# Kernel tuning notes

Hardware: AMD Instinct MI355X
Metric: run time of the kernel (lower is better)

Reference implementation:

```python
import jax, jax.numpy as jnp
import numpy as np

DICT_LEN = 9
NUM_LS = 8
DIM = 1024
SEQ = 2048
BZ = 32


def setup_inputs() -> dict:
    key = jax.random.key(0)
    k_x, k_ids, k_w, k_b = jax.random.split(key, 4)
    x = jax.random.normal(k_x, (SEQ, BZ, DIM), dtype=jnp.float32)
    lang_ids = jax.random.randint(k_ids, (BZ,), 0, DICT_LEN)
    # torch nn.Linear init: U(-1/sqrt(in), 1/sqrt(in)), weight shape [out, in]
    bound = 1.0 / np.sqrt(DIM)
    W = jax.random.uniform(k_w, (NUM_LS, DIM, DIM), dtype=jnp.float32, minval=-bound, maxval=bound)
    b = jax.random.uniform(k_b, (NUM_LS, DIM), dtype=jnp.float32, minval=-bound, maxval=bound)
    return {"x": x, "lang_ids": lang_ids, "W": W, "b": b}


def reference(x, lang_ids, W, b):
    # Mapper.forward: gid = dict_len - 1 - lang_ids; tokens with gid in [1, num_ls]
    # are transformed by Linear #(gid-1); all other batch columns pass through.
    gid = DICT_LEN - 1 - lang_ids                      # [bz]
    active = (gid >= 1) & (gid <= NUM_LS)              # [bz]
    eidx = jnp.clip(gid - 1, 0, NUM_LS - 1)            # [bz] expert index (dummy 0 where inactive)
    We = W[eidx]                                       # [bz, dim, dim] (torch Linear weight layout [out, in])
    be = b[eidx]                                       # [bz, dim]
    y = jnp.einsum("sbd,bed->sbe", x, We) + be[None, :, :]
    return jnp.where(active[None, :, None], y, x)
```

## Files before the change

### kernel.cpp

```cpp
#include <hip/hip_runtime.h>
#include <hip/hip_bf16.h>

#define TSEQ 2048
#define TBZ  32
#define TDIM 1024
#define NLS  8

typedef __attribute__((ext_vector_type(8))) short bf16x8;
typedef __attribute__((ext_vector_type(4))) float f32x4;

__device__ inline unsigned int pk2(float lo, float hi) {
    __hip_bfloat162 h = __float22bfloat162_rn(make_float2(lo, hi));
    return *reinterpret_cast<const unsigned int*>(&h);
}

__device__ inline void gload_lds16(const void* g, void* l) {
    __builtin_amdgcn_global_load_lds(
        (const __attribute__((address_space(1))) unsigned int*)g,
        (__attribute__((address_space(3))) unsigned int*)l,
        16, 0, 0);
}

__global__ __launch_bounds__(256) void conv_x(
    const float* __restrict__ x, const int* __restrict__ lang_ids,
    unsigned short* __restrict__ xb, float* __restrict__ out)
{
    const int b   = blockIdx.x >> 5;
    const int s0c = (blockIdx.x & 31) * 64;
    const int gid = 8 - lang_ids[b];
    const bool active = (gid >= 1) && (gid <= 8);

    for (int i = threadIdx.x; i < 64 * 128; i += 256) {
        const int ls = i >> 7;
        const int d8 = i & 127;
        const int s  = s0c + ls;
        const float* src = x + ((long)s * TBZ + b) * TDIM + d8 * 8;
        f32x4 v0 = *(const f32x4*)(src);
        f32x4 v1 = *(const f32x4*)(src + 4);
        if (active) {
            uint4 o;
            o.x = pk2(v0.x, v0.y); o.y = pk2(v0.z, v0.w);
            o.z = pk2(v1.x, v1.y); o.w = pk2(v1.z, v1.w);
            *(uint4*)(xb + ((long)b * TSEQ + s) * TDIM + d8 * 8) = o;
        } else {
            float* dst = out + ((long)s * TBZ + b) * TDIM + d8 * 8;
            *(f32x4*)(dst)     = v0;
            *(f32x4*)(dst + 4) = v1;
        }
    }
}

__global__ __launch_bounds__(256) void conv_w(const float* __restrict__ W,
                                              unsigned short* __restrict__ wb) {
    const int total = NLS * TDIM * TDIM / 8;
    const int stride = gridDim.x * 256;
    for (int i = blockIdx.x * 256 + threadIdx.x; i < total; i += stride) {
        const float* src = W + (long)i * 8;
        f32x4 v0 = *(const f32x4*)(src);
        f32x4 v1 = *(const f32x4*)(src + 4);
        uint4 o;
        o.x = pk2(v0.x, v0.y); o.y = pk2(v0.z, v0.w);
        o.z = pk2(v1.x, v1.y); o.w = pk2(v1.z, v1.w);
        *(uint4*)(wb + (long)i * 8) = o;
    }
}


#define BAR __builtin_amdgcn_s_barrier()
#define LGKM asm volatile("s_waitcnt lgkmcnt(0)" ::: "memory")
#define VMC(n) asm volatile("s_waitcnt vmcnt(" #n ")" ::: "memory")
#define KAo(kv) (((kv) & 1023) + (((kv) >> 10) << 18))
#define KBo(kv) ((kv) & 1023)

__global__ __launch_bounds__(512, 2) void mapper_gemm8p(
    const unsigned short* __restrict__ xb,
    const int* __restrict__ lang_ids,
    const unsigned short* __restrict__ wb,
    const float* __restrict__ bias,
    float* __restrict__ out)
{
    const int p  = blockIdx.x;
    const int l  = (p & 7) * 32 + (p >> 3);
    const int b  = l >> 3;
    const int strip = (l >> 2) & 1;
    const int nt = l & 3;
    const int s0 = strip * 1024;
    const int e0 = nt * 256;
    const int tid = threadIdx.x;

    const int gid = 8 - lang_ids[b];
    if (!(gid >= 1 && gid <= 8)) return;
    const int eb = gid - 1;

    __shared__ uint4 ldsbuf[131072 / 16];
    char* ldsc = (char*)ldsbuf;

    const int lane = tid & 63;
    const int wave = tid >> 6;
    const int wr   = wave >> 2;
    const int wc   = wave & 3;
    const int fr   = lane & 15;
    const int fq   = lane >> 4;
    const int fr7  = fr & 7;

    const unsigned short* __restrict__ Aab = xb + (long)b  * TSEQ * TDIM + (long)s0 * TDIM;
    const unsigned short* __restrict__ Bbb = wb + (long)eb * TDIM * TDIM + (long)e0 * TDIM;

    const int L    = lane;
    const int lch8 = ((L & 7) ^ (L >> 3)) * 8;
    const int ldA0 = wave * 2048 + L * 16;
    const unsigned short* aG[2][2];
    const unsigned short* bG[2][2];
    #pragma unroll
    for (int j = 0; j < 2; ++j) {
        const int rr = wave * 16 + j * 8 + (L >> 3);
        #pragma unroll
        for (int mh = 0; mh < 2; ++mh)
            aG[j][mh] = Aab + ((rr >> 6) * 128 + mh * 64 + (rr & 63)) * TDIM + lch8;
        #pragma unroll
        for (int nh = 0; nh < 2; ++nh)
            bG[j][nh] = Bbb + ((rr >> 5) * 64 + nh * 32 + (rr & 31)) * TDIM + lch8;
    }

#define STAGE_A(slot, mh, kofs) do { \
    gload_lds16(aG[0][mh] + (kofs), ldsc + (slot)*32768 + (mh)*16384 + ldA0); \
    gload_lds16(aG[1][mh] + (kofs), ldsc + (slot)*32768 + (mh)*16384 + ldA0 + 1024); \
} while (0)
#define STAGE_B(slot, nh, kofs) do { \
    gload_lds16(bG[0][nh] + (kofs), ldsc + 65536 + (slot)*32768 + (nh)*16384 + ldA0); \
    gload_lds16(bG[1][nh] + (kofs), ldsc + 65536 + (slot)*32768 + (nh)*16384 + ldA0 + 1024); \
} while (0)
#define RD_A(slot, mh) do { \
    _Pragma("unroll") for (int ml = 0; ml < 4; ++ml) { \
        const int rr = wr * 64 + ml * 16 + fr; \
        _Pragma("unroll") for (int kk = 0; kk < 2; ++kk) \
            af[ml][kk] = *(const bf16x8*)(ldsc + (slot)*32768 + (mh)*16384 + rr*128 + (((kk*4+fq) ^ fr7) << 4)); \
    } } while (0)
#define RD_B(slot, nh, br) do { \
    _Pragma("unroll") for (int nl = 0; nl < 2; ++nl) { \
        const int rr = wc * 32 + nl * 16 + fr; \
        _Pragma("unroll") for (int kk = 0; kk < 2; ++kk) \
            br[nl][kk] = *(const bf16x8*)(ldsc + 65536 + (slot)*32768 + (nh)*16384 + rr*128 + (((kk*4+fq) ^ fr7) << 4)); \
    } } while (0)
#define MM(mh, nh, br) do { \
    __builtin_amdgcn_s_setprio(1); \
    _Pragma("unroll") for (int ml = 0; ml < 4; ++ml) \
    _Pragma("unroll") for (int nl = 0; nl < 2; ++nl) \
    _Pragma("unroll") for (int kk = 0; kk < 2; ++kk) \
        acc[(mh)*4+ml][(nh)*2+nl] = __builtin_amdgcn_mfma_f32_16x16x32_bf16( \
            br[nl][kk], af[ml][kk], acc[(mh)*4+ml][(nh)*2+nl], 0, 0, 0); \
    __builtin_amdgcn_s_setprio(0); \
} while (0)

    f32x4 acc[8][4];
    #pragma unroll
    for (int m = 0; m < 8; ++m)
        #pragma unroll
        for (int n = 0; n < 4; ++n)
            acc[m][n] = (f32x4){0.f, 0.f, 0.f, 0.f};

    bf16x8 af[4][2], bf0[2][2], bf1[2][2];

    STAGE_A(0, 0, 0);  STAGE_B(0, 0, 0);  STAGE_B(0, 1, 0);  STAGE_A(0, 1, 0);
    STAGE_A(1, 0, 64); STAGE_B(1, 0, 64); STAGE_B(1, 1, 64);
    VMC(6); BAR;

    const int cs  = lane & 15;
    const int eqb = (lane >> 4) << 2;

    for (int mtl = 0; mtl < 4; ++mtl) {
        for (int it = 0; it < 8; ++it) {
            const int kva = mtl * 1024 + it * 128;
            const int kb = kva + 64;
            const int kn = kva + 128;
            const int km = kva + 192;
            RD_A(0, 0); RD_B(0, 0, bf0); STAGE_A(1, 1, KAo(kb));
            BAR; LGKM; MM(0, 0, bf0); BAR;
            RD_B(0, 1, bf1); STAGE_A(0, 0, KAo(kn));
            BAR; LGKM; MM(0, 1, bf1); BAR;
            RD_A(0, 1); STAGE_B(0, 0, KBo(kn));
            BAR; LGKM; MM(1, 0, bf0); BAR;
            STAGE_B(0, 1, KBo(kn));
            BAR; MM(1, 1, bf1); VMC(6); BAR;
            RD_A(1, 0); RD_B(1, 0, bf0); STAGE_A(0, 1, KAo(kn));
            BAR; LGKM; MM(0, 0, bf0); BAR;
            RD_B(1, 1, bf1); STAGE_A(1, 0, KAo(km));
            BAR; LGKM; MM(0, 1, bf1); BAR;
            RD_A(1, 1); STAGE_B(1, 0, KBo(km));
            BAR; LGKM; MM(1, 0, bf0); BAR;
            STAGE_B(1, 1, KBo(km));
            BAR; MM(1, 1, bf1); VMC(6); BAR;
        }

        const int sb = s0 + mtl * 256 + wr * 128;
        #pragma unroll
        for (int n = 0; n < 4; ++n) {
            const int e = e0 + wc * 64 + n * 16 + eqb;
            const f32x4 bv4 = *(const f32x4*)&bias[eb * TDIM + e];
            #pragma unroll
            for (int m = 0; m < 8; ++m) {
                const int s = sb + m * 16 + cs;
                *(f32x4*)&out[(long)s * (TBZ * TDIM) + b * TDIM + e] = acc[m][n] + bv4;
            }
        }
        #pragma unroll
        for (int m = 0; m < 8; ++m)
            #pragma unroll
            for (int n = 0; n < 4; ++n)
                acc[m][n] = (f32x4){0.f, 0.f, 0.f, 0.f};
    }
#undef STAGE_A
#undef STAGE_B
#undef RD_A
#undef RD_B
#undef MM
}

__device__ inline unsigned short f2bf(float f) {
    union { float f; unsigned int u; } v; v.f = f;
    unsigned int r = v.u + 0x7fffu + ((v.u >> 16) & 1u);
    return (unsigned short)(r >> 16);
}
constexpr int FLDS = 40;

__global__ __launch_bounds__(256) void mapper_fused(
    const float* __restrict__ x, const int* __restrict__ lang_ids,
    const float* __restrict__ W, const float* __restrict__ bias,
    float* __restrict__ out)
{
    const int bid = blockIdx.x;
    const int b   = bid >> 7;
    const int t   = bid & 127;
    const int mt  = t >> 3;
    const int nt  = t & 7;
    const int s0  = mt * 128;
    const int e0  = nt * 128;
    const int tid = threadIdx.x;

    const int gid = 8 - lang_ids[b];
    const bool active = (gid >= 1) && (gid <= 8);
    int eb = gid - 1; eb = eb < 0 ? 0 : (eb > 7 ? 7 : eb);

    if (!active) {
        const f32x4* xs = (const f32x4*)x;
        f32x4*       os = (f32x4*)out;
        const int rs4 = TBZ * TDIM / 4;
        for (int i = tid; i < 128 * 128 / 4; i += 256) {
            int r = i >> 5, c = i & 31;
            long idx = (long)(s0 + r) * rs4 + b * (TDIM / 4) + (e0 >> 2) + c;
            os[idx] = xs[idx];
        }
        return;
    }

    __shared__ unsigned short As[128 * FLDS];
    __shared__ unsigned short Bs[128 * FLDS];
    const float* __restrict__ Wb = W + (long)eb * TDIM * TDIM;

    const int lane = tid & 63;
    const int wave = tid >> 6;
    const int wrr  = wave >> 1;
    const int wcc  = wave & 1;

    f32x4 acc[4][4];
    #pragma unroll
    for (int m = 0; m < 4; ++m)
        #pragma unroll
        for (int n = 0; n < 4; ++n)
            acc[m][n] = (f32x4){0.f, 0.f, 0.f, 0.f};

    const int rg = tid >> 3;
    const int cg = tid & 7;
    const int fr = lane & 15;
    const int fo = (lane >> 4) * 8;

    for (int k0 = 0; k0 < TDIM; k0 += 32) {
        __syncthreads();
        #pragma unroll
        for (int pp = 0; pp < 4; ++pp) {
            const int r = rg + pp * 32;
            f32x4 av = *(const f32x4*)(x  + (long)(s0 + r) * (TBZ * TDIM) + b * TDIM + k0 + cg * 4);
            f32x4 bv = *(const f32x4*)(Wb + (long)(e0 + r) * TDIM + k0 + cg * 4);
            unsigned int alo = (unsigned)f2bf(av.x) | ((unsigned)f2bf(av.y) << 16);
            unsigned int ahi = (unsigned)f2bf(av.z) | ((unsigned)f2bf(av.w) << 16);
            unsigned int blo = (unsigned)f2bf(bv.x) | ((unsigned)f2bf(bv.y) << 16);
            unsigned int bhi = (unsigned)f2bf(bv.z) | ((unsigned)f2bf(bv.w) << 16);
            *(uint2*)&As[r * FLDS + cg * 4] = make_uint2(alo, ahi);
            *(uint2*)&Bs[r * FLDS + cg * 4] = make_uint2(blo, bhi);
        }
        __syncthreads();

        bf16x8 af2[4], bfm[4];
        #pragma unroll
        for (int m = 0; m < 4; ++m)
            af2[m] = *(const bf16x8*)&As[(wrr * 64 + m * 16 + fr) * FLDS + fo];
        #pragma unroll
        for (int n = 0; n < 4; ++n)
            bfm[n] = *(const bf16x8*)&Bs[(wcc * 64 + n * 16 + fr) * FLDS + fo];
        #pragma unroll
        for (int m = 0; m < 4; ++m)
            #pragma unroll
            for (int n = 0; n < 4; ++n)
                acc[m][n] = __builtin_amdgcn_mfma_f32_16x16x32_bf16(af2[m], bfm[n], acc[m][n], 0, 0, 0);
    }

    const int cr = lane >> 4;
    const int cc2 = lane & 15;
    #pragma unroll
    for (int n = 0; n < 4; ++n) {
        const int e  = e0 + wcc * 64 + n * 16 + cc2;
        const float bv = bias[eb * TDIM + e];
        #pragma unroll
        for (int m = 0; m < 4; ++m) {
            #pragma unroll
            for (int j = 0; j < 4; ++j) {
                const int s = s0 + wrr * 64 + m * 16 + cr * 4 + j;
                out[(long)s * (TBZ * TDIM) + b * TDIM + e] = acc[m][n][j] + bv;
            }
        }
    }
}

extern "C" void kernel_launch(void* const* d_in, const int* in_sizes, int n_in,
                              void* d_out, int out_size, void* d_ws, size_t ws_size,
                              hipStream_t stream) {
    const float* x        = (const float*)d_in[0];
    const int*   lang_ids = (const int*)d_in[1];
    const float* W        = (const float*)d_in[2];
    const float* bias     = (const float*)d_in[3];
    float*       out      = (float*)d_out;

    const size_t xbytes = (size_t)TSEQ * TBZ * TDIM * 2;
    const size_t wbytes = (size_t)NLS * TDIM * TDIM * 2;

    if (ws_size >= xbytes + wbytes) {
        unsigned short* xbp = (unsigned short*)d_ws;
        unsigned short* wbp = (unsigned short*)((char*)d_ws + xbytes);
        conv_x<<<1024, 256, 0, stream>>>(x, lang_ids, xbp, out);
        conv_w<<<2048, 256, 0, stream>>>(W, wbp);
        mapper_gemm8p<<<256, 512, 0, stream>>>(xbp, lang_ids, wbp, bias, out);
    } else {
        mapper_fused<<<TBZ * 16 * 8, 256, 0, stream>>>(x, lang_ids, W, bias, out);
    }
}
```

Baseline: 265.9 us.

## Merge conversion kernels and replace explicit lgkmcnt waits with sched barriers

The x and W bf16 conversion kernels become one launch, with 256 blocks converting W and 2048 smaller blocks handling x, which removes a kernel launch boundary. In the GEMM main loop the explicit s_waitcnt lgkmcnt(0) before each MFMA group is dropped and sched_barrier(0) fences are added so the compiler inserts the waits and cannot reorder across phases. This may reduce stall time, but it depends on the compiler placing the LDS-read waits correctly.

```diff
diff --git a/kernel.cpp b/kernel.cpp
--- a/kernel.cpp
+++ b/kernel.cpp
@@ -21,16 +21,33 @@
         16, 0, 0);
 }
 
-__global__ __launch_bounds__(256) void conv_x(
+__global__ __launch_bounds__(256) void conv_all(
     const float* __restrict__ x, const int* __restrict__ lang_ids,
-    unsigned short* __restrict__ xb, float* __restrict__ out)
+    const float* __restrict__ W,
+    unsigned short* __restrict__ xb, unsigned short* __restrict__ wb,
+    float* __restrict__ out)
 {
-    const int b   = blockIdx.x >> 5;
-    const int s0c = (blockIdx.x & 31) * 64;
-    const int gid = 8 - lang_ids[b];
+    const int bid = blockIdx.x;
+    if (bid < 256) {
+        const int total = NLS * TDIM * TDIM / 8;
+        for (int i = bid * 256 + threadIdx.x; i < total; i += 256 * 256) {
+            const float* src = W + (long)i * 8;
+            f32x4 v0 = *(const f32x4*)(src);
+            f32x4 v1 = *(const f32x4*)(src + 4);
+            uint4 o;
+            o.x = pk2(v0.x, v0.y); o.y = pk2(v0.z, v0.w);
+            o.z = pk2(v1.x, v1.y); o.w = pk2(v1.z, v1.w);
+            *(uint4*)(wb + (long)i * 8) = o;
+        }
+        return;
+    }
+    const int xb_id = bid - 256;
+    const int b     = xb_id >> 6;
+    const int s0c   = (xb_id & 63) * 32;
+    const int gid   = 8 - lang_ids[b];
     const bool active = (gid >= 1) && (gid <= 8);
 
-    for (int i = threadIdx.x; i < 64 * 128; i += 256) {
+    for (int i = threadIdx.x; i < 32 * 128; i += 256) {
         const int ls = i >> 7;
         const int d8 = i & 127;
         const int s  = s0c + ls;
@@ -50,24 +67,9 @@
     }
 }
 
-__global__ __launch_bounds__(256) void conv_w(const float* __restrict__ W,
-                                              unsigned short* __restrict__ wb) {
-    const int total = NLS * TDIM * TDIM / 8;
-    const int stride = gridDim.x * 256;
-    for (int i = blockIdx.x * 256 + threadIdx.x; i < total; i += stride) {
-        const float* src = W + (long)i * 8;
-        f32x4 v0 = *(const f32x4*)(src);
-        f32x4 v1 = *(const f32x4*)(src + 4);
-        uint4 o;
-        o.x = pk2(v0.x, v0.y); o.y = pk2(v0.z, v0.w);
-        o.z = pk2(v1.x, v1.y); o.w = pk2(v1.z, v1.w);
-        *(uint4*)(wb + (long)i * 8) = o;
-    }
-}
-
 
 #define BAR __builtin_amdgcn_s_barrier()
-#define LGKM asm volatile("s_waitcnt lgkmcnt(0)" ::: "memory")
+#define SB0 __builtin_amdgcn_sched_barrier(0)
 #define VMC(n) asm volatile("s_waitcnt vmcnt(" #n ")" ::: "memory")
 #define KAo(kv) (((kv) & 1023) + (((kv) >> 10) << 18))
 #define KBo(kv) ((kv) & 1023)
@@ -163,7 +165,7 @@
 
     STAGE_A(0, 0, 0);  STAGE_B(0, 0, 0);  STAGE_B(0, 1, 0);  STAGE_A(0, 1, 0);
     STAGE_A(1, 0, 64); STAGE_B(1, 0, 64); STAGE_B(1, 1, 64);
-    VMC(6); BAR;
+    VMC(6); BAR; SB0;
 
     const int cs  = lane & 15;
     const int eqb = (lane >> 4) << 2;
@@ -175,21 +177,21 @@
             const int kn = kva + 128;
             const int km = kva + 192;
             RD_A(0, 0); RD_B(0, 0, bf0); STAGE_A(1, 1, KAo(kb));
-            BAR; LGKM; MM(0, 0, bf0); BAR;
+            BAR; SB0; MM(0, 0, bf0); BAR; SB0;
             RD_B(0, 1, bf1); STAGE_A(0, 0, KAo(kn));
-            BAR; LGKM; MM(0, 1, bf1); BAR;
+            BAR; SB0; MM(0, 1, bf1); BAR; SB0;
             RD_A(0, 1); STAGE_B(0, 0, KBo(kn));
-            BAR; LGKM; MM(1, 0, bf0); BAR;
+            BAR; SB0; MM(1, 0, bf0); BAR; SB0;
             STAGE_B(0, 1, KBo(kn));
-            BAR; MM(1, 1, bf1); VMC(6); BAR;
+            BAR; SB0; MM(1, 1, bf1); VMC(6); BAR; SB0;
             RD_A(1, 0); RD_B(1, 0, bf0); STAGE_A(0, 1, KAo(kn));
-            BAR; LGKM; MM(0, 0, bf0); BAR;
+            BAR; SB0; MM(0, 0, bf0); BAR; SB0;
             RD_B(1, 1, bf1); STAGE_A(1, 0, KAo(km));
-            BAR; LGKM; MM(0, 1, bf1); BAR;
+            BAR; SB0; MM(0, 1, bf1); BAR; SB0;
             RD_A(1, 1); STAGE_B(1, 0, KBo(km));
-            BAR; LGKM; MM(1, 0, bf0); BAR;
+            BAR; SB0; MM(1, 0, bf0); BAR; SB0;
             STAGE_B(1, 1, KBo(km));
-            BAR; MM(1, 1, bf1); VMC(6); BAR;
+            BAR; SB0; MM(1, 1, bf1); VMC(6); BAR; SB0;
         }
 
         const int sb = s0 + mtl * 256 + wr * 128;
@@ -336,8 +338,7 @@
     if (ws_size >= xbytes + wbytes) {
         unsigned short* xbp = (unsigned short*)d_ws;
         unsigned short* wbp = (unsigned short*)((char*)d_ws + xbytes);
-        conv_x<<<1024, 256, 0, stream>>>(x, lang_ids, xbp, out);
-        conv_w<<<2048, 256, 0, stream>>>(W, wbp);
+        conv_all<<<2304, 256, 0, stream>>>(x, lang_ids, W, xbp, wbp, out);
         mapper_gemm8p<<<256, 512, 0, stream>>>(xbp, lang_ids, wbp, bias, out);
     } else {
         mapper_fused<<<TBZ * 16 * 8, 256, 0, stream>>>(x, lang_ids, W, bias, out);
```

Result: no change. 261.5 us (-1.7%).
